# Kernel optimization log

Hardware: AMD Instinct MI355X
Metric: run time of the kernel (lower is better)

The kernel has to match this reference:

```python
import jax, jax.numpy as jnp
import numpy as np

B, L, D, H = 4, 8192, 512, 8


def _phi(x):
    # feature map: elu(x) + 1 (strictly positive)
    return jax.nn.elu(x) + 1.0


def setup_inputs() -> dict:
    key = jax.random.key(0)
    k1, k2, k3 = jax.random.split(key, 3)
    x = jax.random.normal(k1, (B, L, D), dtype=jnp.float32)
    w_qkv = jax.random.normal(k2, (D, 3 * D), dtype=jnp.float32) * 0.02
    b_qkv = jnp.zeros((3 * D,), dtype=jnp.float32)
    w_out = jax.random.normal(k3, (D, D), dtype=jnp.float32) * 0.02
    b_out = jnp.zeros((D,), dtype=jnp.float32)
    return {"x": x, "w_qkv": w_qkv, "b_qkv": b_qkv, "w_out": w_out,
            "b_out": b_out, "num_heads": H}


def reference(x, w_qkv, b_qkv, w_out, b_out, num_heads):
    Bx, Lx, Dx = x.shape
    dh = Dx // num_heads
    qkv = x @ w_qkv + b_qkv                       # (B, L, 3D)
    q, k, v = jnp.split(qkv, 3, axis=-1)
    # (B, L, D) -> (B, H, L, dh)
    def to_heads(t):
        return t.reshape(Bx, Lx, num_heads, dh).transpose(0, 2, 1, 3)
    q = _phi(to_heads(q))
    k = _phi(to_heads(k))
    v = to_heads(v)
    # kv[b,h,m,d] = sum_l k[b,h,l,d] * v[b,h,l,m]
    kv = jnp.einsum('bhld,bhlm->bhmd', k, v)      # (B, H, dh, dh)
    k_sum = jnp.sum(k, axis=2, keepdims=True)     # (B, H, 1, dh)
    # z[b,h,l,1] = 1 / <q_l, k_sum + 1e-6>
    z = 1.0 / jnp.einsum('bhld,bhmd->bhlm', q, k_sum + 1e-6)  # (B,H,L,1)
    out = jnp.einsum('bhld,bhmd->bhlm', q, kv) * z            # (B,H,L,dh)
    out = out.transpose(0, 2, 1, 3).reshape(Bx, Lx, Dx)
    return out @ w_out + b_out
```

## Files before the change

kernel.cpp:

```cpp
#include <hip/hip_runtime.h>
#include <hip/hip_bf16.h>
#include <math.h>

#define BB 4
#define LL 8192
#define DD 512
#define HH 8
#define MM (BB*LL)
#define NQKV 1536
#define CH 16

typedef __attribute__((ext_vector_type(4))) float f32x4;
typedef __attribute__((ext_vector_type(8))) short s16x8;
typedef __attribute__((ext_vector_type(4))) short s16x4;

__device__ __forceinline__ float bf2f(short u) {
  union { unsigned int i; float f; } c;
  c.i = ((unsigned int)(unsigned short)u) << 16;
  return c.f;
}
__device__ __forceinline__ short f2bf(float f) {
  union { float f; unsigned int i; } c; c.f = f;
  unsigned int r = c.i + 0x7FFFu + ((c.i >> 16) & 1u);
  return (short)(r >> 16);
}

__device__ __forceinline__ void gload16(const void* g, void* l) {
  __builtin_amdgcn_global_load_lds(
      (const __attribute__((address_space(1))) void*)(g),
      (__attribute__((address_space(3))) void*)(l), 16, 0, 0);
}

__global__ void conv_bf16(const float* __restrict__ in, short* __restrict__ out, int n) {
  int i = (blockIdx.x * blockDim.x + threadIdx.x) * 8;
  if (i < n) {
    float4 v0 = *reinterpret_cast<const float4*>(in + i);
    float4 v1 = *reinterpret_cast<const float4*>(in + i + 4);
    s16x8 o;
    o[0] = f2bf(v0.x); o[1] = f2bf(v0.y); o[2] = f2bf(v0.z); o[3] = f2bf(v0.w);
    o[4] = f2bf(v1.x); o[5] = f2bf(v1.y); o[6] = f2bf(v1.z); o[7] = f2bf(v1.w);
    *reinterpret_cast<s16x8*>(out + i) = o;
  }
}

__global__ void conv_wt(const float* __restrict__ w, short* __restrict__ wt, int K, int N) {
  int idx = blockIdx.x * blockDim.x + threadIdx.x;
  if (idx < K * N) {
    int n = idx / K, k = idx - n * K;
    wt[idx] = f2bf(w[(size_t)k * N + n]);
  }
}

__global__ __launch_bounds__(512, 4)
void gemm_bt(const short* __restrict__ A, const short* __restrict__ BT,
             const float* __restrict__ bias, void* __restrict__ Cout,
             short* __restrict__ ktb, short* __restrict__ vtb)
{
  constexpr int KD = 512;
  __shared__ __align__(16) char lds[65536];

  const int tid = threadIdx.x;
  const int wv = tid >> 6, lane = tid & 63;
  const int wm = wv >> 1, wn = wv & 1;
  const int fr = lane & 15, fq = lane >> 4;

  const int gx = gridDim.x;
  const int gy = gridDim.y;
  const int d = blockIdx.y * gx + blockIdx.x;
  const int nwg = gx * gy;
  const int lin = (d & 7) * (nwg >> 3) + (d >> 3);
  const int m0 = (lin / gy) * 256, n0 = (lin % gy) * 128;

  const int srow = tid >> 3;
  const int sunit = (tid & 7) ^ (srow & 7);
  const short* Ag = A  + (size_t)(m0 + srow) * KD + sunit * 8;
  const short* Bg = BT + (size_t)(n0 + srow) * KD + sunit * 8;
  char* ldsw = lds + wv * 1024;

  f32x4 acc[4][4] = {};

  for (int t = 0; t < 8; ++t) {
    const int k0 = t * 64;
#pragma unroll
    for (int i = 0; i < 4; ++i)
      gload16(Ag + (size_t)(i * 64) * KD + k0, ldsw + i * 8192);
#pragma unroll
    for (int i = 0; i < 2; ++i)
      gload16(Bg + (size_t)(i * 64) * KD + k0, ldsw + 32768 + i * 8192);
    __syncthreads();
#pragma unroll
    for (int kk = 0; kk < 2; ++kk) {
      s16x8 af[4], bfg[4];
#pragma unroll
      for (int i = 0; i < 4; ++i) {
        const int ra = wm * 64 + i * 16 + fr;
        const int ua = (kk * 4 + fq) ^ (ra & 7);
        af[i] = *(const s16x8*)(lds + ra * 128 + ua * 16);
      }
#pragma unroll
      for (int j = 0; j < 4; ++j) {
        const int rb = wn * 64 + j * 16 + fr;
        const int ub = (kk * 4 + fq) ^ (rb & 7);
        bfg[j] = *(const s16x8*)(lds + 32768 + rb * 128 + ub * 16);
      }
#pragma unroll
      for (int i = 0; i < 4; ++i)
#pragma unroll
        for (int j = 0; j < 4; ++j)
          acc[i][j] = __builtin_amdgcn_mfma_f32_16x16x32_bf16(af[i], bfg[j], acc[i][j], 0, 0, 0);
    }
    __syncthreads();
  }

  if (n0 < 512) {
    short* scr = (short*)lds;
#pragma unroll
    for (int j = 0; j < 4; ++j) {
      const int col = wn * 64 + j * 16 + fr;
      const float bv = bias[n0 + col];
#pragma unroll
      for (int i = 0; i < 4; ++i) {
        const int row = wm * 64 + i * 16 + fq * 4;
#pragma unroll
        for (int r = 0; r < 4; ++r) {
          float v = acc[i][j][r] + bv;
          v = (v > 0.f) ? (v + 1.f) : __expf(v);
          scr[(row + r) * 128 + col] = f2bf(v);
        }
      }
    }
    __syncthreads();
#pragma unroll
    for (int p = 0; p < 8; ++p) {
      const int off = p * 8192 + tid * 16;
      const int row = off >> 8, colb = off & 255;
      s16x8 v = *(const s16x8*)(lds + off);
      *(s16x8*)((short*)Cout + (size_t)(m0 + row) * 512 + n0 + (colb >> 1)) = v;
    }
  } else {
    const bool do_phi = (n0 < 1024);
    short* tdst = do_phi ? ktb : vtb;
    const int f0 = n0 - (do_phi ? 512 : 1024);
#pragma unroll
    for (int j = 0; j < 4; ++j) {
      const int col = wn * 64 + j * 16 + fr;
      const float bv = bias[n0 + col];
      const int cx = col & 31;
#pragma unroll
      for (int i = 0; i < 4; ++i) {
        const int l = wm * 64 + i * 16 + fq * 4;
        s16x4 pk;
#pragma unroll
        for (int r = 0; r < 4; ++r) {
          float v = acc[i][j][r] + bv;
          if (do_phi) v = (v > 0.f) ? (v + 1.f) : __expf(v);
          pk[r] = f2bf(v);
        }
        *(s16x4*)(lds + col * 512 + (((l >> 3) ^ cx) * 16) + (l & 7) * 2) = pk;
      }
    }
    __syncthreads();
#pragma unroll
    for (int p = 0; p < 8; ++p) {
      const int g = p * 512 + tid;
      const int col = g >> 5, up = g & 31;
      const int u = up ^ (col & 31);
      s16x8 v = *(const s16x8*)(lds + col * 512 + up * 16);
      const int f = f0 + col;
      const int hb = ((m0 >> 13) << 3) + (f >> 6);
      short* dst = tdst + ((size_t)hb * 64 + (f & 63)) * 8192 + (m0 & 8191) + u * 8;
      *(s16x8*)dst = v;
    }
  }
}

__global__ __launch_bounds__(256, 4)
void kv_mfma(const short* __restrict__ kt, const short* __restrict__ vt,
             float* __restrict__ pkv, float* __restrict__ pks)
{
  const int hb = blockIdx.x, c = blockIdx.y;
  const int tid = threadIdx.x, wv = tid >> 6, lane = tid & 63;
  const int fr = lane & 15, fq = lane >> 4;
  const size_t base = (size_t)hb * 64 * 8192;
  const int l0 = c * 512;
  const short* vrow = vt + base + (size_t)fr * 8192 + l0 + fq * 8;
  const short* krow = kt + base + (size_t)(wv * 16 + fr) * 8192 + l0 + fq * 8;

  s16x8 ones;
#pragma unroll
  for (int j = 0; j < 8; ++j) ones[j] = (short)0x3F80;

  f32x4 acc[4] = {};
  f32x4 accd = {};
#pragma unroll
  for (int ks = 0; ks < 16; ++ks) {
    s16x8 bfr = *(const s16x8*)(krow + ks * 32);
    accd = __builtin_amdgcn_mfma_f32_16x16x32_bf16(ones, bfr, accd, 0, 0, 0);
#pragma unroll
    for (int i = 0; i < 4; ++i) {
      s16x8 af = *(const s16x8*)(vrow + (size_t)(i * 16) * 8192 + ks * 32);
      acc[i] = __builtin_amdgcn_mfma_f32_16x16x32_bf16(af, bfr, acc[i], 0, 0, 0);
    }
  }
  float* o = pkv + ((size_t)hb * CH + c) * 4096;
#pragma unroll
  for (int i = 0; i < 4; ++i)
#pragma unroll
    for (int r = 0; r < 4; ++r)
      o[(i * 16 + fq * 4 + r) * 64 + wv * 16 + fr] = acc[i][r];
  if (fq == 0)
    pks[((size_t)hb * CH + c) * 64 + wv * 16 + fr] = accd[0];
}

__global__ void kv_reduce(const float* __restrict__ pkv, const float* __restrict__ pks,
                          short* __restrict__ kv_b, short* __restrict__ ksum_b)
{
  const int idx = blockIdx.x * 256 + threadIdx.x;
  const int head = idx >> 12, md = idx & 4095;
  float s = 0.f;
  for (int i = 0; i < CH; ++i) s += pkv[((size_t)head * CH + i) * 4096 + md];
  kv_b[idx] = f2bf(s);
  if (md < 64) {
    float t = 0.f;
    for (int i = 0; i < CH; ++i) t += pks[((size_t)head * CH + i) * 64 + md];
    ksum_b[head * 64 + md] = f2bf(t + 1e-6f);
  }
}

__global__ __launch_bounds__(256, 2)
void attn_out(const short* __restrict__ q_b, const short* __restrict__ kv_b,
              const short* __restrict__ ksum_b, const short* __restrict__ wo_t,
              const float* __restrict__ b_out, float* __restrict__ out)
{
  __shared__ __align__(16) char lds[73728];
  const int tid = threadIdx.x;
  const int wv = tid >> 6, lane = tid & 63;
  const int fr = lane & 15, fq = lane >> 4;
  const int l0 = blockIdx.x * 64;
  const int bb = l0 >> 13;

  const int srow = tid >> 3;
  const int sunit = (tid & 7) ^ (srow & 7);
  const short* Wg = wo_t + (size_t)srow * 512 + sunit * 8;
  char* ldsw = lds + 8192 + wv * 1024;

  f32x4 acc[4][8] = {};

  for (int h = 0; h < 8; ++h) {
#pragma unroll
    for (int i = 0; i < 16; ++i)
      gload16(Wg + (size_t)(i * 32) * 512 + h * 64, ldsw + i * 4096);

    {
      const int hb = bb * 8 + h;
      const short* kvp = kv_b + (size_t)hb * 4096;
      const short* ksp = ksum_b + hb * 64;
      const short* qb = q_b + (size_t)(l0 + wv * 16) * 512 + h * 64;
      f32x4 accn[4] = {};
      f32x4 accd = {};
#pragma unroll
      for (int kk = 0; kk < 2; ++kk) {
        s16x8 a = *(const s16x8*)(qb + (size_t)fr * 512 + kk * 32 + fq * 8);
        s16x8 bden = *(const s16x8*)(ksp + kk * 32 + fq * 8);
        accd = __builtin_amdgcn_mfma_f32_16x16x32_bf16(a, bden, accd, 0, 0, 0);
#pragma unroll
        for (int j = 0; j < 4; ++j) {
          s16x8 bfr = *(const s16x8*)(kvp + (j * 16 + fr) * 64 + kk * 32 + fq * 8);
          accn[j] = __builtin_amdgcn_mfma_f32_16x16x32_bf16(a, bfr, accn[j], 0, 0, 0);
        }
      }
#pragma unroll
      for (int r = 0; r < 4; ++r) {
        const int row = wv * 16 + fq * 4 + r;
        const float dinv = 1.0f / accd[r];
#pragma unroll
        for (int j = 0; j < 4; ++j) {
          const int col = j * 16 + fr;
          *(short*)(lds + row * 128 + (((col >> 3) ^ (row & 7)) << 4) + ((col & 7) << 1))
              = f2bf(accn[j][r] * dinv);
        }
      }
    }
    __syncthreads();

#pragma unroll
    for (int kk = 0; kk < 2; ++kk) {
      s16x8 af[4];
#pragma unroll
      for (int i = 0; i < 4; ++i) {
        const int row = i * 16 + fr;
        const int u = (kk * 4 + fq) ^ (row & 7);
        af[i] = *(const s16x8*)(lds + row * 128 + u * 16);
      }
#pragma unroll
      for (int j = 0; j < 8; ++j) {
        const int n = wv * 128 + j * 16 + fr;
        const int u = (kk * 4 + fq) ^ (n & 7);
        s16x8 bw = *(const s16x8*)(lds + 8192 + n * 128 + u * 16);
#pragma unroll
        for (int i = 0; i < 4; ++i)
          acc[i][j] = __builtin_amdgcn_mfma_f32_16x16x32_bf16(af[i], bw, acc[i][j], 0, 0, 0);
      }
    }
    __syncthreads();
  }

  float* scrf = (float*)lds;
#pragma unroll
  for (int p = 0; p < 2; ++p) {
#pragma unroll
    for (int ii = 0; ii < 2; ++ii) {
      const int i = 2 * p + ii;
#pragma unroll
      for (int j = 0; j < 8; ++j) {
        const int col = wv * 128 + j * 16 + fr;
        const float bv = b_out[col];
#pragma unroll
        for (int r = 0; r < 4; ++r)
          scrf[(ii * 16 + fq * 4 + r) * 512 + col] = acc[i][j][r] + bv;
      }
    }
    __syncthreads();
#pragma unroll
    for (int pp = 0; pp < 16; ++pp) {
      const int off = pp * 4096 + tid * 16;
      const int row = off >> 11, colb = off & 2047;
      float4 v = *(const float4*)(lds + off);
      *(float4*)(out + (size_t)(l0 + p * 32 + row) * 512 + (colb >> 2)) = v;
    }
    __syncthreads();
  }
}

extern "C" void kernel_launch(void* const* d_in, const int* in_sizes, int n_in,
                              void* d_out, int out_size, void* d_ws, size_t ws_size,
                              hipStream_t stream)
{
  const float* x     = (const float*)d_in[0];
  const float* w_qkv = (const float*)d_in[1];
  const float* b_qkv = (const float*)d_in[2];
  const float* w_out = (const float*)d_in[3];
  const float* b_out = (const float*)d_in[4];

  char* ws = (char*)d_ws;
  size_t off = 0;
  short* x_b   = (short*)(ws + off); off += (size_t)MM * DD * 2;
  short* wq_t  = (short*)(ws + off); off += (size_t)NQKV * DD * 2;
  short* wo_t  = (short*)(ws + off); off += (size_t)DD * DD * 2;
  short* q_b   = (short*)(ws + off); off += (size_t)MM * DD * 2;
  short* kt    = (short*)(ws + off); off += (size_t)32 * 64 * LL * 2;
  short* vt    = (short*)(ws + off); off += (size_t)32 * 64 * LL * 2;
  float* pkv   = (float*)(ws + off); off += (size_t)32 * CH * 4096 * 4;
  float* pks   = (float*)(ws + off); off += (size_t)32 * CH * 64 * 4;
  short* kv_b  = (short*)(ws + off); off += (size_t)32 * 4096 * 2;
  short* ksum_b= (short*)(ws + off); off += (size_t)32 * 64 * 2;

  conv_bf16<<<dim3(MM * DD / 8 / 256), dim3(256), 0, stream>>>(x, x_b, MM * DD);
  conv_wt<<<dim3((DD * NQKV + 255) / 256), dim3(256), 0, stream>>>(w_qkv, wq_t, DD, NQKV);
  conv_wt<<<dim3((DD * DD + 255) / 256), dim3(256), 0, stream>>>(w_out, wo_t, DD, DD);

  gemm_bt<<<dim3(MM / 256, NQKV / 128), dim3(512), 0, stream>>>(
      x_b, wq_t, b_qkv, (void*)q_b, kt, vt);

  kv_mfma<<<dim3(32, CH), dim3(256), 0, stream>>>(kt, vt, pkv, pks);
  kv_reduce<<<dim3(512), dim3(256), 0, stream>>>(pkv, pks, kv_b, ksum_b);

  attn_out<<<dim3(MM / 64), dim3(256), 0, stream>>>(
      q_b, kv_b, ksum_b, wo_t, b_out, (float*)d_out);
}
```

Before: 164.9 us.

## Fuse conversion kernels and enlarge attn_out tile to 128 rows with 8 waves

The three fp32-to-bf16 conversion launches are merged into one kernel that dispatches on block index, removing two launches. attn_out now processes 128 rows per block with 512 threads in a 2x4 wave grid, so each W_out tile loaded into LDS is reused across twice as many rows. This halves W_out global traffic per row but raises LDS use to 80KB per block, which may limit occupancy. The output staging loop is reorganised to match.

```diff
diff --git a/kernel.cpp b/kernel.cpp
--- a/kernel.cpp
+++ b/kernel.cpp
@@ -31,23 +31,27 @@
       (__attribute__((address_space(3))) void*)(l), 16, 0, 0);
 }
 
-__global__ void conv_bf16(const float* __restrict__ in, short* __restrict__ out, int n) {
-  int i = (blockIdx.x * blockDim.x + threadIdx.x) * 8;
-  if (i < n) {
-    float4 v0 = *reinterpret_cast<const float4*>(in + i);
-    float4 v1 = *reinterpret_cast<const float4*>(in + i + 4);
+__global__ void conv_all(const float* __restrict__ x, const float* __restrict__ wq,
+                         const float* __restrict__ wo, short* __restrict__ x_b,
+                         short* __restrict__ wq_t, short* __restrict__ wo_t)
+{
+  const int b = blockIdx.x, tid = threadIdx.x;
+  if (b < 8192) {
+    const int i = (b * 256 + tid) * 8;
+    float4 v0 = *reinterpret_cast<const float4*>(x + i);
+    float4 v1 = *reinterpret_cast<const float4*>(x + i + 4);
     s16x8 o;
     o[0] = f2bf(v0.x); o[1] = f2bf(v0.y); o[2] = f2bf(v0.z); o[3] = f2bf(v0.w);
     o[4] = f2bf(v1.x); o[5] = f2bf(v1.y); o[6] = f2bf(v1.z); o[7] = f2bf(v1.w);
-    *reinterpret_cast<s16x8*>(out + i) = o;
-  }
-}
-
-__global__ void conv_wt(const float* __restrict__ w, short* __restrict__ wt, int K, int N) {
-  int idx = blockIdx.x * blockDim.x + threadIdx.x;
-  if (idx < K * N) {
-    int n = idx / K, k = idx - n * K;
-    wt[idx] = f2bf(w[(size_t)k * N + n]);
+    *reinterpret_cast<s16x8*>(x_b + i) = o;
+  } else if (b < 11264) {
+    const int idx = (b - 8192) * 256 + tid;
+    const int n = idx >> 9, k = idx & 511;
+    wq_t[idx] = f2bf(wq[(size_t)k * NQKV + n]);
+  } else {
+    const int idx = (b - 11264) * 256 + tid;
+    const int n = idx >> 9, k = idx & 511;
+    wo_t[idx] = f2bf(wo[(size_t)k * DD + n]);
   }
 }
 
@@ -64,8 +68,7 @@
   const int wm = wv >> 1, wn = wv & 1;
   const int fr = lane & 15, fq = lane >> 4;
 
-  const int gx = gridDim.x;
-  const int gy = gridDim.y;
+  const int gx = gridDim.x, gy = gridDim.y;
   const int d = blockIdx.y * gx + blockIdx.x;
   const int nwg = gx * gy;
   const int lin = (d & 7) * (nwg >> 3) + (d >> 3);
@@ -227,29 +230,29 @@
   }
 }
 
-__global__ __launch_bounds__(256, 2)
+__global__ __launch_bounds__(512, 2)
 void attn_out(const short* __restrict__ q_b, const short* __restrict__ kv_b,
               const short* __restrict__ ksum_b, const short* __restrict__ wo_t,
               const float* __restrict__ b_out, float* __restrict__ out)
 {
-  __shared__ __align__(16) char lds[73728];
+  __shared__ __align__(16) char lds[81920];
   const int tid = threadIdx.x;
   const int wv = tid >> 6, lane = tid & 63;
   const int fr = lane & 15, fq = lane >> 4;
-  const int l0 = blockIdx.x * 64;
+  const int l0 = blockIdx.x * 128;
   const int bb = l0 >> 13;
 
   const int srow = tid >> 3;
   const int sunit = (tid & 7) ^ (srow & 7);
   const short* Wg = wo_t + (size_t)srow * 512 + sunit * 8;
-  char* ldsw = lds + 8192 + wv * 1024;
+  char* ldsw = lds + 16384 + wv * 1024;
 
   f32x4 acc[4][8] = {};
 
   for (int h = 0; h < 8; ++h) {
 #pragma unroll
-    for (int i = 0; i < 16; ++i)
-      gload16(Wg + (size_t)(i * 32) * 512 + h * 64, ldsw + i * 4096);
+    for (int i = 0; i < 8; ++i)
+      gload16(Wg + (size_t)(i * 64) * 512 + h * 64, ldsw + i * 8192);
 
     {
       const int hb = bb * 8 + h;
@@ -283,20 +286,21 @@
     }
     __syncthreads();
 
+    const int wm2 = wv >> 2, wn2 = wv & 3;
 #pragma unroll
     for (int kk = 0; kk < 2; ++kk) {
       s16x8 af[4];
 #pragma unroll
       for (int i = 0; i < 4; ++i) {
-        const int row = i * 16 + fr;
+        const int row = wm2 * 64 + i * 16 + fr;
         const int u = (kk * 4 + fq) ^ (row & 7);
         af[i] = *(const s16x8*)(lds + row * 128 + u * 16);
       }
 #pragma unroll
       for (int j = 0; j < 8; ++j) {
-        const int n = wv * 128 + j * 16 + fr;
+        const int n = wn2 * 128 + j * 16 + fr;
         const int u = (kk * 4 + fq) ^ (n & 7);
-        s16x8 bw = *(const s16x8*)(lds + 8192 + n * 128 + u * 16);
+        s16x8 bw = *(const s16x8*)(lds + 16384 + n * 128 + u * 16);
 #pragma unroll
         for (int i = 0; i < 4; ++i)
           acc[i][j] = __builtin_amdgcn_mfma_f32_16x16x32_bf16(af[i], bw, acc[i][j], 0, 0, 0);
@@ -305,25 +309,28 @@
     __syncthreads();
   }
 
+  const int wm2 = wv >> 2, wn2 = wv & 3;
   float* scrf = (float*)lds;
 #pragma unroll
-  for (int p = 0; p < 2; ++p) {
-#pragma unroll
-    for (int ii = 0; ii < 2; ++ii) {
-      const int i = 2 * p + ii;
-#pragma unroll
-      for (int j = 0; j < 8; ++j) {
-        const int col = wv * 128 + j * 16 + fr;
-        const float bv = b_out[col];
-#pragma unroll
-        for (int r = 0; r < 4; ++r)
-          scrf[(ii * 16 + fq * 4 + r) * 512 + col] = acc[i][j][r] + bv;
-      }
-    }
-    __syncthreads();
-#pragma unroll
-    for (int pp = 0; pp < 16; ++pp) {
-      const int off = pp * 4096 + tid * 16;
+  for (int p = 0; p < 4; ++p) {
+    if (wm2 == (p >> 1)) {
+#pragma unroll
+      for (int ii = 0; ii < 2; ++ii) {
+        const int i = (p & 1) * 2 + ii;
+#pragma unroll
+        for (int j = 0; j < 8; ++j) {
+          const int col = wn2 * 128 + j * 16 + fr;
+          const float bv = b_out[col];
+#pragma unroll
+          for (int r = 0; r < 4; ++r)
+            scrf[(ii * 16 + fq * 4 + r) * 512 + col] = acc[i][j][r] + bv;
+        }
+      }
+    }
+    __syncthreads();
+#pragma unroll
+    for (int pp = 0; pp < 8; ++pp) {
+      const int off = pp * 8192 + tid * 16;
       const int row = off >> 11, colb = off & 2047;
       float4 v = *(const float4*)(lds + off);
       *(float4*)(out + (size_t)(l0 + p * 32 + row) * 512 + (colb >> 2)) = v;
@@ -355,9 +362,7 @@
   short* kv_b  = (short*)(ws + off); off += (size_t)32 * 4096 * 2;
   short* ksum_b= (short*)(ws + off); off += (size_t)32 * 64 * 2;
 
-  conv_bf16<<<dim3(MM * DD / 8 / 256), dim3(256), 0, stream>>>(x, x_b, MM * DD);
-  conv_wt<<<dim3((DD * NQKV + 255) / 256), dim3(256), 0, stream>>>(w_qkv, wq_t, DD, NQKV);
-  conv_wt<<<dim3((DD * DD + 255) / 256), dim3(256), 0, stream>>>(w_out, wo_t, DD, DD);
+  conv_all<<<dim3(12288), dim3(256), 0, stream>>>(x, w_qkv, w_out, x_b, wq_t, wo_t);
 
   gemm_bt<<<dim3(MM / 256, NQKV / 128), dim3(512), 0, stream>>>(
       x_b, wq_t, b_qkv, (void*)q_b, kt, vt);
@@ -365,6 +370,6 @@
   kv_mfma<<<dim3(32, CH), dim3(256), 0, stream>>>(kt, vt, pkv, pks);
   kv_reduce<<<dim3(512), dim3(256), 0, stream>>>(pkv, pks, kv_b, ksum_b);
 
-  attn_out<<<dim3(MM / 64), dim3(256), 0, stream>>>(
+  attn_out<<<dim3(MM / 128), dim3(512), 0, stream>>>(
       q_b, kv_b, ksum_b, wo_t, b_out, (float*)d_out);
 }
```

Result: no change. 162.9 us (-1.2%).
